# Optimization experiments

Hardware: AMD Instinct MI355X
Metric: run time of the kernel (lower is better)

The kernel has to match this reference:

```python
import jax, jax.numpy as jnp
import numpy as np

N = 131072        # combined nodes (dst + relabeled src)
E = 1048576       # combined edges
NUM_DST = 65536   # block.num_dst_nodes(dst_ntype)
IN_DIM = 256
HEADS = 4
OUT = 32
NEG_SLOPE = 0.2   # DGL GATConv leaky_relu default
N_DST_RELS = 2    # relations targeting dst_ntype


def setup_inputs() -> dict:
    key = jax.random.key(0)
    ks = jax.random.split(key, 6)
    feats = jax.random.normal(ks[0], (N, IN_DIM), dtype=jnp.float32)
    src = jax.random.randint(ks[1], (E,), 0, N, dtype=jnp.int32)
    dst = jax.random.randint(ks[2], (E,), 0, NUM_DST, dtype=jnp.int32)
    scale = 1.0 / np.sqrt(IN_DIM)
    W = jax.random.normal(ks[3], (IN_DIM, HEADS * OUT), dtype=jnp.float32) * scale
    attn_l = jax.random.normal(ks[4], (HEADS, OUT), dtype=jnp.float32) * 0.1
    attn_r = jax.random.normal(ks[5], (HEADS, OUT), dtype=jnp.float32) * 0.1
    return {"feats": feats, "src": src, "dst": dst, "W": W,
            "attn_l": attn_l, "attn_r": attn_r, "num_dst": NUM_DST}


def reference(feats, src, dst, W, attn_l, attn_r, num_dst):
    # GATConv (eval mode: dropout = identity), allow_zero_in_degree=True.
    h = (feats @ W).reshape(N, HEADS, OUT)                 # [N,H,D] projected feats
    el = jnp.einsum('nhd,hd->nh', h, attn_l)               # [N,H] src attn logits
    er = jnp.einsum('nhd,hd->nh', h, attn_r)               # [N,H] dst attn logits
    e = jax.nn.leaky_relu(el[src] + er[dst], NEG_SLOPE)    # [E,H]
    # edge softmax per dst node (all dst < num_dst; z[num_dst:] is discarded anyway)
    emax = jax.ops.segment_max(e, dst, num_segments=NUM_DST)     # [num_dst,H]
    ee = jnp.exp(e - emax[dst])
    esum = jax.ops.segment_sum(ee, dst, num_segments=NUM_DST)
    alpha = ee / esum[dst]                                 # [E,H]
    msg = h[src] * alpha[..., None]                        # [E,H,D]
    rst = jax.ops.segment_sum(msg, dst, num_segments=NUM_DST)    # [num_dst,H,D]
    dst_z = jax.nn.elu(rst).reshape(NUM_DST, HEADS * OUT)  # activation=F.elu, flatten(1)
    att_sc = jnp.ones((N_DST_RELS,), dtype=jnp.float32)
    return dst_z, att_sc
```

## Files before the change

### kernel.cpp

```cpp
#include <hip/hip_runtime.h>
#include <hip/hip_fp16.h>
#include <math.h>

#define N_NODES 131072
#define E_EDGES 1048576
#define NDST    65536
#define NEG_SLOPE 0.2f
#define MAXDEG  64
#define NBUCK   1024
#define DPB     64
#define BCAP    1248
#define BIN_BLOCKS 128

typedef __attribute__((ext_vector_type(8))) short short8;
typedef __attribute__((ext_vector_type(4))) float f32x4;

__device__ __forceinline__ unsigned short f2bf(float f) {
    unsigned u = __float_as_uint(f);
    u = (u + 0x7fffu + ((u >> 16) & 1u)) >> 16;
    return (unsigned short)u;
}
__device__ __forceinline__ __half2 u2h2(unsigned u) {
    union { unsigned u; __half2 h; } c; c.u = u; return c.h;
}
__device__ __forceinline__ unsigned h22u(__half2 h) {
    union { __half2 h; unsigned u; } c; c.h = h; return c.u;
}

__global__ void prep_w(const float* __restrict__ W, unsigned short* __restrict__ Wt,
                       int* __restrict__ gcur) {
    int idx = blockIdx.x * 256 + threadIdx.x;
    if (idx < NBUCK) gcur[idx] = 0;
    int k = idx >> 7, n = idx & 127;
    Wt[n * 256 + k] = f2bf(W[idx]);
}

__global__ __launch_bounds__(512, 4) void gemm_bin(const float* __restrict__ A,
                                                   const unsigned short* __restrict__ Wt,
                                                   const float* __restrict__ attn_l,
                                                   const float* __restrict__ attn_r,
                                                   unsigned short* __restrict__ hout,
                                                   float* __restrict__ el,
                                                   float* __restrict__ er,
                                                   const int* __restrict__ src,
                                                   const int* __restrict__ dst,
                                                   int* __restrict__ gcur,
                                                   unsigned* __restrict__ ebuf) {
    __shared__ unsigned short lds[16384];
    const int t = threadIdx.x;

    if (blockIdx.x < BIN_BLOCKS) {
        int* lh  = (int*)lds;
        int* lb  = lh + NBUCK;
        int* lh2 = lb + NBUCK;
        const int e0 = (blockIdx.x * 512 + t) * 16;
        int4 sv[4], dv[4];
#pragma unroll
        for (int i = 0; i < 4; ++i) {
            sv[i] = *(const int4*)(src + e0 + i * 4);
            dv[i] = *(const int4*)(dst + e0 + i * 4);
        }
        const int* s = (const int*)sv;
        const int* d = (const int*)dv;
        for (int i = t; i < NBUCK; i += 512) lh[i] = 0;
        __syncthreads();
#pragma unroll
        for (int k = 0; k < 16; ++k) atomicAdd(&lh[d[k] >> 6], 1);
        __syncthreads();
        for (int i = t; i < NBUCK; i += 512) {
            int c = lh[i];
            lb[i] = c ? atomicAdd(&gcur[i], c) : 0;
            lh2[i] = 0;
        }
        __syncthreads();
#pragma unroll
        for (int k = 0; k < 16; ++k) {
            int bk = d[k] >> 6;
            int r = lb[bk] + atomicAdd(&lh2[bk], 1);
            if (r < BCAP) ebuf[(size_t)bk * BCAP + r] = ((unsigned)s[k] << 6) | (unsigned)(d[k] & 63);
        }
        return;
    }

    const int w  = t >> 6, l = t & 63;
    const int n  = l & 15, kq = l >> 4;
    const int wm = w & 1,  wn = w >> 1;
    const size_t m0 = (size_t)(blockIdx.x - BIN_BLOCKS) * 64;

    short8 bfr[2][8];
    const unsigned short* wb = Wt + (size_t)(wn * 32 + n) * 256 + kq * 8;
#pragma unroll
    for (int nj = 0; nj < 2; ++nj)
#pragma unroll
        for (int s = 0; s < 8; ++s)
            bfr[nj][s] = *(const short8*)(wb + nj * 16 * 256 + s * 32);

    const float4* gsrc = (const float4*)(A + m0 * 256);
#pragma unroll
    for (int batch = 0; batch < 2; ++batch) {
        float4 tmp[4];
#pragma unroll
        for (int i = 0; i < 4; ++i) tmp[i] = gsrc[(batch * 4 + i) * 512 + t];
#pragma unroll
        for (int i = 0; i < 4; ++i) {
            int f   = (batch * 4 + i) * 512 + t;
            int row = f >> 6, c4 = f & 63;
            unsigned lo = (unsigned)f2bf(tmp[i].x) | ((unsigned)f2bf(tmp[i].y) << 16);
            unsigned hi = (unsigned)f2bf(tmp[i].z) | ((unsigned)f2bf(tmp[i].w) << 16);
            unsigned byte = (unsigned)(row * 512) + (((unsigned)(c4 * 8)) ^ (((unsigned)(row & 7)) << 4));
            *(uint2*)((char*)lds + byte) = make_uint2(lo, hi);
        }
    }
    __syncthreads();

    f32x4 acc[2][2];
#pragma unroll
    for (int mi = 0; mi < 2; ++mi)
#pragma unroll
        for (int nj = 0; nj < 2; ++nj) acc[mi][nj] = (f32x4){0.f, 0.f, 0.f, 0.f};

#pragma unroll
    for (int s = 0; s < 8; ++s) {
        short8 af[2];
#pragma unroll
        for (int mi = 0; mi < 2; ++mi) {
            int row = wm * 32 + mi * 16 + n;
            unsigned byte = (unsigned)(row * 512) +
                            (((unsigned)(s * 64 + kq * 16)) ^ (((unsigned)(row & 7)) << 4));
            af[mi] = *(const short8*)((char*)lds + byte);
        }
#pragma unroll
        for (int nj = 0; nj < 2; ++nj)
#pragma unroll
            for (int mi = 0; mi < 2; ++mi)
                acc[mi][nj] = __builtin_amdgcn_mfma_f32_16x16x32_bf16(af[mi], bfr[nj][s],
                                                                      acc[mi][nj], 0, 0, 0);
    }

    float al[2], ar[2];
#pragma unroll
    for (int nj = 0; nj < 2; ++nj) {
        al[nj] = attn_l[wn * 32 + nj * 16 + n];
        ar[nj] = attn_r[wn * 32 + nj * 16 + n];
    }
    float pl[2][4], pr[2][4];
#pragma unroll
    for (int mi = 0; mi < 2; ++mi)
#pragma unroll
        for (int i = 0; i < 4; ++i) {
            pl[mi][i] = acc[mi][0][i] * al[0] + acc[mi][1][i] * al[1];
            pr[mi][i] = acc[mi][0][i] * ar[0] + acc[mi][1][i] * ar[1];
        }
#pragma unroll
    for (int m = 1; m < 16; m <<= 1)
#pragma unroll
        for (int mi = 0; mi < 2; ++mi)
#pragma unroll
            for (int i = 0; i < 4; ++i) {
                pl[mi][i] += __shfl_xor(pl[mi][i], m);
                pr[mi][i] += __shfl_xor(pr[mi][i], m);
            }
    if (n == 0) {
#pragma unroll
        for (int mi = 0; mi < 2; ++mi)
#pragma unroll
            for (int i = 0; i < 4; ++i) {
                size_t row = m0 + wm * 32 + mi * 16 + kq * 4 + i;
                el[row * 4 + wn] = pl[mi][i];
                if (row < NDST) er[row * 4 + wn] = pr[mi][i];
            }
    }

    __syncthreads();
    unsigned short* scr = lds;
#pragma unroll
    for (int mi = 0; mi < 2; ++mi)
#pragma unroll
        for (int nj = 0; nj < 2; ++nj)
#pragma unroll
            for (int i = 0; i < 4; ++i)
                scr[(wm * 32 + mi * 16 + kq * 4 + i) * 136 + wn * 32 + nj * 16 + n] =
                    __half_as_ushort(__float2half(acc[mi][nj][i]));
    __syncthreads();
#pragma unroll
    for (int j = 0; j < 2; ++j) {
        int c = j * 512 + t;
        int row = c >> 4, sub = c & 15;
        short8 v = *(const short8*)(scr + row * 136 + sub * 8);
        *(short8*)(hout + (m0 + row) * 128 + sub * 8) = v;
    }
}

__global__ __launch_bounds__(512, 4) void agg_fused(const int* __restrict__ gcur,
                                                    const unsigned* __restrict__ ebuf,
                                                    const float* __restrict__ el,
                                                    const float* __restrict__ er,
                                                    const char* __restrict__ h,
                                                    float* __restrict__ out) {
    __shared__ int lcnt[DPB];
    __shared__ int lcsr[DPB * MAXDEG];
    __shared__ __align__(16) char stag[8 * 1536];
    const int t = threadIdx.x;
    const int w = t >> 6, lane = t & 63;
    const int b = blockIdx.x;
    if (b == 0 && t < 2) out[(size_t)NDST * 128 + t] = 1.0f;

    if (t < DPB) lcnt[t] = 0;
    __syncthreads();
    int nb = gcur[b]; if (nb > BCAP) nb = BCAP;
    for (int i = t; i < nb; i += 512) {
        unsigned e = ebuf[(size_t)b * BCAP + i];
        int dloc = e & 63;
        int pos = atomicAdd(&lcnt[dloc], 1);
        if (pos < MAXDEG) lcsr[dloc * MAXDEG + pos] = (int)(e >> 6);
    }
    __syncthreads();

    char* pbase = &stag[w * 1536];
    char* sbase = pbase + 1024;
    const int g = lane >> 4, q = lane & 15, head = q >> 2;
    const unsigned qoff = (unsigned)q * 16;

#pragma unroll 1
    for (int rep = 0; rep < 8; ++rep) {
        int dloc = (w << 3) + rep;
        int wid = b * DPB + dloc;
        int deg = lcnt[dloc]; if (deg > MAXDEG) deg = MAXDEG;
        float4 er4 = *(const float4*)(er + (size_t)wid * 4);

        bool valid = lane < deg;
        int s = valid ? lcsr[dloc * MAXDEG + lane] : 0;
        float4 ev = *(const float4*)(el + (size_t)s * 4);
        ev.x += er4.x; ev.y += er4.y; ev.z += er4.z; ev.w += er4.w;
        ev.x = ev.x > 0.f ? ev.x : NEG_SLOPE * ev.x;
        ev.y = ev.y > 0.f ? ev.y : NEG_SLOPE * ev.y;
        ev.z = ev.z > 0.f ? ev.z : NEG_SLOPE * ev.z;
        ev.w = ev.w > 0.f ? ev.w : NEG_SLOPE * ev.w;
        float4 p;
        p.x = valid ? __expf(ev.x) : 0.f;
        p.y = valid ? __expf(ev.y) : 0.f;
        p.z = valid ? __expf(ev.z) : 0.f;
        p.w = valid ? __expf(ev.w) : 0.f;

        float4 ss = p;
#pragma unroll
        for (int m = 1; m < 64; m <<= 1) {
            ss.x += __shfl_xor(ss.x, m);
            ss.y += __shfl_xor(ss.y, m);
            ss.z += __shfl_xor(ss.z, m);
            ss.w += __shfl_xor(ss.w, m);
        }

        if (valid) {
            uint4 pk;
            pk.x = h22u(__float2half2_rn(p.x));
            pk.y = h22u(__float2half2_rn(p.y));
            pk.z = h22u(__float2half2_rn(p.z));
            pk.w = h22u(__float2half2_rn(p.w));
            *(uint4*)(pbase + lane * 16) = pk;
            *(unsigned*)(sbase + lane * 4) = ((unsigned)s) << 8;
        }

        __half2 acc0 = u2h2(0), acc1 = u2h2(0), acc2 = u2h2(0), acc3 = u2h2(0);
        int it = (deg > g) ? ((deg - g + 3) >> 2) : 0;
        const char* pa = pbase + g * 16 + head * 4;
        const char* sa = sbase + g * 4;

        unsigned pp0 = 0, pp1 = 0;
        uint4 hv0 = make_uint4(0, 0, 0, 0), hv1 = make_uint4(0, 0, 0, 0);
        if (it > 0) {
            pp0 = *(const unsigned*)pa;
            hv0 = *(const uint4*)(h + *(const unsigned*)sa + qoff);
        }
        if (it > 1) {
            pp1 = *(const unsigned*)(pa + 64);
            hv1 = *(const uint4*)(h + *(const unsigned*)(sa + 16) + qoff);
        }
#pragma unroll 1
        for (int j = 2; j < it; ++j) {
            unsigned npp = *(const unsigned*)(pa + (size_t)j * 64);
            unsigned ns  = *(const unsigned*)(sa + (size_t)j * 16);
            uint4 nhv = *(const uint4*)(h + ns + qoff);
            __half2 pA = u2h2(pp0);
            acc0 = __hfma2(u2h2(hv0.x), pA, acc0);
            acc1 = __hfma2(u2h2(hv0.y), pA, acc1);
            acc2 = __hfma2(u2h2(hv0.z), pA, acc2);
            acc3 = __hfma2(u2h2(hv0.w), pA, acc3);
            pp0 = pp1; hv0 = hv1;
            pp1 = npp; hv1 = nhv;
        }
        {
            __half2 pA = u2h2(pp0), pB = u2h2(pp1);
            acc0 = __hfma2(u2h2(hv0.x), pA, acc0);
            acc1 = __hfma2(u2h2(hv0.y), pA, acc1);
            acc2 = __hfma2(u2h2(hv0.z), pA, acc2);
            acc3 = __hfma2(u2h2(hv0.w), pA, acc3);
            acc0 = __hfma2(u2h2(hv1.x), pB, acc0);
            acc1 = __hfma2(u2h2(hv1.y), pB, acc1);
            acc2 = __hfma2(u2h2(hv1.z), pB, acc2);
            acc3 = __hfma2(u2h2(hv1.w), pB, acc3);
        }

        float2 f0 = __half22float2(acc0);
        float2 f1 = __half22float2(acc1);
        float2 f2 = __half22float2(acc2);
        float2 f3 = __half22float2(acc3);
        float fa[8] = {f0.x, f0.y, f1.x, f1.y, f2.x, f2.y, f3.x, f3.y};
#pragma unroll
        for (int m = 16; m < 64; m <<= 1)
#pragma unroll
            for (int k = 0; k < 8; ++k) fa[k] += __shfl_xor(fa[k], m);

        if (g == 0) {
            float slo  = (head & 1) ? ss.y : ss.x;
            float shi  = (head & 1) ? ss.w : ss.z;
            float ssel = (head & 2) ? shi : slo;
            float inv  = ssel > 0.f ? 1.0f / ssel : 0.f;
            float o[8];
#pragma unroll
            for (int k = 0; k < 8; ++k) {
                float v = fa[k] * inv;
                o[k] = v > 0.f ? v : expm1f(v);
            }
            float* op = out + (size_t)wid * 128 + q * 8;
            *(float4*)(op)     = make_float4(o[0], o[1], o[2], o[3]);
            *(float4*)(op + 4) = make_float4(o[4], o[5], o[6], o[7]);
        }
    }
}

extern "C" void kernel_launch(void* const* d_in, const int* in_sizes, int n_in,
                              void* d_out, int out_size, void* d_ws, size_t ws_size,
                              hipStream_t stream) {
    const float* feats  = (const float*)d_in[0];
    const int*   src    = (const int*)d_in[1];
    const int*   dst    = (const int*)d_in[2];
    const float* W      = (const float*)d_in[3];
    const float* attn_l = (const float*)d_in[4];
    const float* attn_r = (const float*)d_in[5];
    float* out = (float*)d_out;

    char* base = (char*)d_ws;
    unsigned short* h_16 = (unsigned short*)base;
    size_t off = (size_t)N_NODES * 128 * 2;
    unsigned short* Wt = (unsigned short*)(base + off); off += 65536;
    float* el  = (float*)(base + off); off += (size_t)N_NODES * 4 * 4;
    float* er  = (float*)(base + off); off += (size_t)NDST * 4 * 4;
    int*   gcur = (int*)(base + off);  off += (size_t)NBUCK * 4;
    unsigned* ebuf = (unsigned*)(base + off);

    prep_w<<<128, 256, 0, stream>>>(W, Wt, gcur);
    gemm_bin<<<BIN_BLOCKS + N_NODES / 64, 512, 0, stream>>>(feats, Wt, attn_l, attn_r,
                                                            h_16, el, er, src, dst, gcur, ebuf);
    agg_fused<<<NBUCK, 512, 0, stream>>>(gcur, ebuf, el, er, (const char*)h_16, out);
}
```

Baseline: 116.2 us.

## Store projected features head-major and aggregate one head at a time

The projection kernel now writes h in a head-major layout [head][node][32], so each head's features for a node occupy 64 contiguous bytes. The aggregation loop iterates heads serially, with 16 edges processed in parallel per wave and 4 lanes per edge covering 32 features. This shrinks each gather to a 64-byte segment per edge and raises edge-level parallelism, but runs 4 head passes that each re-read the index list. The cross-lane reduction is now done in half precision, which may cost accuracy.

```diff
diff --git a/kernel.cpp b/kernel.cpp
--- a/kernel.cpp
+++ b/kernel.cpp
@@ -185,9 +185,11 @@
 #pragma unroll
     for (int j = 0; j < 2; ++j) {
         int c = j * 512 + t;
-        int row = c >> 4, sub = c & 15;
-        short8 v = *(const short8*)(scr + row * 136 + sub * 8);
-        *(short8*)(hout + (m0 + row) * 128 + sub * 8) = v;
+        int hh  = c >> 8;
+        int row = (c >> 2) & 63;
+        int sub = c & 3;
+        short8 v = *(const short8*)(scr + row * 136 + hh * 32 + sub * 8);
+        *(short8*)(hout + ((size_t)hh * N_NODES + (m0 + row)) * 32 + sub * 8) = v;
     }
 }
 
@@ -218,8 +220,8 @@
 
     char* pbase = &stag[w * 1536];
     char* sbase = pbase + 1024;
-    const int g = lane >> 4, q = lane & 15, head = q >> 2;
-    const unsigned qoff = (unsigned)q * 16;
+    const int es = lane >> 2, qq = lane & 3;
+    const unsigned qoff = (unsigned)qq * 16;
 
 #pragma unroll 1
     for (int rep = 0; rep < 8; ++rep) {
@@ -251,80 +253,91 @@
             ss.w += __shfl_xor(ss.w, m);
         }
 
+        uint4 pk = make_uint4(0, 0, 0, 0);
+        unsigned sv = 0;
         if (valid) {
-            uint4 pk;
             pk.x = h22u(__float2half2_rn(p.x));
             pk.y = h22u(__float2half2_rn(p.y));
             pk.z = h22u(__float2half2_rn(p.z));
             pk.w = h22u(__float2half2_rn(p.w));
-            *(uint4*)(pbase + lane * 16) = pk;
-            *(unsigned*)(sbase + lane * 4) = ((unsigned)s) << 8;
-        }
-
-        __half2 acc0 = u2h2(0), acc1 = u2h2(0), acc2 = u2h2(0), acc3 = u2h2(0);
-        int it = (deg > g) ? ((deg - g + 3) >> 2) : 0;
-        const char* pa = pbase + g * 16 + head * 4;
-        const char* sa = sbase + g * 4;
-
-        unsigned pp0 = 0, pp1 = 0;
-        uint4 hv0 = make_uint4(0, 0, 0, 0), hv1 = make_uint4(0, 0, 0, 0);
-        if (it > 0) {
-            pp0 = *(const unsigned*)pa;
-            hv0 = *(const uint4*)(h + *(const unsigned*)sa + qoff);
-        }
-        if (it > 1) {
-            pp1 = *(const unsigned*)(pa + 64);
-            hv1 = *(const uint4*)(h + *(const unsigned*)(sa + 16) + qoff);
-        }
+            sv = ((unsigned)s) << 6;
+        }
+        *(uint4*)(pbase + lane * 16) = pk;
+        *(unsigned*)(sbase + lane * 4) = sv;
+
+        float inv0 = ss.x > 0.f ? 1.0f / ss.x : 0.f;
+        float inv1 = ss.y > 0.f ? 1.0f / ss.y : 0.f;
+        float inv2 = ss.z > 0.f ? 1.0f / ss.z : 0.f;
+        float inv3 = ss.w > 0.f ? 1.0f / ss.w : 0.f;
+
+        int it = (deg + 15) >> 4;
+
 #pragma unroll 1
-        for (int j = 2; j < it; ++j) {
-            unsigned npp = *(const unsigned*)(pa + (size_t)j * 64);
-            unsigned ns  = *(const unsigned*)(sa + (size_t)j * 16);
-            uint4 nhv = *(const uint4*)(h + ns + qoff);
-            __half2 pA = u2h2(pp0);
-            acc0 = __hfma2(u2h2(hv0.x), pA, acc0);
-            acc1 = __hfma2(u2h2(hv0.y), pA, acc1);
-            acc2 = __hfma2(u2h2(hv0.z), pA, acc2);
-            acc3 = __hfma2(u2h2(hv0.w), pA, acc3);
-            pp0 = pp1; hv0 = hv1;
-            pp1 = npp; hv1 = nhv;
-        }
-        {
-            __half2 pA = u2h2(pp0), pB = u2h2(pp1);
-            acc0 = __hfma2(u2h2(hv0.x), pA, acc0);
-            acc1 = __hfma2(u2h2(hv0.y), pA, acc1);
-            acc2 = __hfma2(u2h2(hv0.z), pA, acc2);
-            acc3 = __hfma2(u2h2(hv0.w), pA, acc3);
-            acc0 = __hfma2(u2h2(hv1.x), pB, acc0);
-            acc1 = __hfma2(u2h2(hv1.y), pB, acc1);
-            acc2 = __hfma2(u2h2(hv1.z), pB, acc2);
-            acc3 = __hfma2(u2h2(hv1.w), pB, acc3);
-        }
-
-        float2 f0 = __half22float2(acc0);
-        float2 f1 = __half22float2(acc1);
-        float2 f2 = __half22float2(acc2);
-        float2 f3 = __half22float2(acc3);
-        float fa[8] = {f0.x, f0.y, f1.x, f1.y, f2.x, f2.y, f3.x, f3.y};
-#pragma unroll
-        for (int m = 16; m < 64; m <<= 1)
-#pragma unroll
-            for (int k = 0; k < 8; ++k) fa[k] += __shfl_xor(fa[k], m);
-
-        if (g == 0) {
-            float slo  = (head & 1) ? ss.y : ss.x;
-            float shi  = (head & 1) ? ss.w : ss.z;
-            float ssel = (head & 2) ? shi : slo;
-            float inv  = ssel > 0.f ? 1.0f / ssel : 0.f;
-            float o[8];
-#pragma unroll
-            for (int k = 0; k < 8; ++k) {
-                float v = fa[k] * inv;
-                o[k] = v > 0.f ? v : expm1f(v);
-            }
-            float* op = out + (size_t)wid * 128 + q * 8;
-            *(float4*)(op)     = make_float4(o[0], o[1], o[2], o[3]);
-            *(float4*)(op + 4) = make_float4(o[4], o[5], o[6], o[7]);
+        for (int hh = 0; hh < 4; ++hh) {
+            const char* hb = h + ((size_t)hh * N_NODES << 6);
+            const char* pa = pbase + es * 16 + hh * 4;
+            const char* sa = sbase + es * 4;
+
+            __half2 a0 = u2h2(0), a1 = u2h2(0), a2 = u2h2(0), a3 = u2h2(0);
+            unsigned pp0 = 0, pp1 = 0;
+            uint4 hv0 = make_uint4(0, 0, 0, 0), hv1 = make_uint4(0, 0, 0, 0);
+            if (it > 0) {
+                pp0 = *(const unsigned*)pa;
+                hv0 = *(const uint4*)(hb + *(const unsigned*)sa + qoff);
+            }
+            if (it > 1) {
+                pp1 = *(const unsigned*)(pa + 256);
+                hv1 = *(const uint4*)(hb + *(const unsigned*)(sa + 64) + qoff);
+            }
+#pragma unroll 1
+            for (int j = 2; j < it; ++j) {
+                unsigned npp = *(const unsigned*)(pa + (size_t)j * 256);
+                unsigned ns  = *(const unsigned*)(sa + (size_t)j * 64);
+                uint4 nhv = *(const uint4*)(hb + ns + qoff);
+                __half2 pA = u2h2(pp0);
+                a0 = __hfma2(u2h2(hv0.x), pA, a0);
+                a1 = __hfma2(u2h2(hv0.y), pA, a1);
+                a2 = __hfma2(u2h2(hv0.z), pA, a2);
+                a3 = __hfma2(u2h2(hv0.w), pA, a3);
+                pp0 = pp1; hv0 = hv1;
+                pp1 = npp; hv1 = nhv;
+            }
+            {
+                __half2 pA = u2h2(pp0), pB = u2h2(pp1);
+                a0 = __hfma2(u2h2(hv0.x), pA, a0);
+                a1 = __hfma2(u2h2(hv0.y), pA, a1);
+                a2 = __hfma2(u2h2(hv0.z), pA, a2);
+                a3 = __hfma2(u2h2(hv0.w), pA, a3);
+                a0 = __hfma2(u2h2(hv1.x), pB, a0);
+                a1 = __hfma2(u2h2(hv1.y), pB, a1);
+                a2 = __hfma2(u2h2(hv1.z), pB, a2);
+                a3 = __hfma2(u2h2(hv1.w), pB, a3);
+            }
+
+#pragma unroll
+            for (int m = 4; m < 64; m <<= 1) {
+                a0 = __hadd2(a0, u2h2(__shfl_xor(h22u(a0), m)));
+                a1 = __hadd2(a1, u2h2(__shfl_xor(h22u(a1), m)));
+                a2 = __hadd2(a2, u2h2(__shfl_xor(h22u(a2), m)));
+                a3 = __hadd2(a3, u2h2(__shfl_xor(h22u(a3), m)));
+            }
+
+            if (es == 0) {
+                float iv = (hh == 0) ? inv0 : (hh == 1) ? inv1 : (hh == 2) ? inv2 : inv3;
+                float2 f0 = __half22float2(a0);
+                float2 f1 = __half22float2(a1);
+                float2 f2 = __half22float2(a2);
+                float2 f3 = __half22float2(a3);
+                float o[8] = {f0.x, f0.y, f1.x, f1.y, f2.x, f2.y, f3.x, f3.y};
+#pragma unroll
+                for (int k = 0; k < 8; ++k) {
+                    float v = o[k] * iv;
+                    o[k] = v > 0.f ? v : expm1f(v);
+                }
+                float* op = out + (size_t)wid * 128 + hh * 32 + qq * 8;
+                *(float4*)(op)     = make_float4(o[0], o[1], o[2], o[3]);
+                *(float4*)(op + 4) = make_float4(o[4], o[5], o[6], o[7]);
+            }
         }
     }
 }
```

After: 166.2 us. 1.43x slower.
